# Performance work log

Hardware: AMD Instinct MI355X
Metric: run time of the kernel (lower is better)

The kernel has to match this reference:

```python
import jax, jax.numpy as jnp
import numpy as np

# dims: N batch, C in-channels, T frames, V joints, H heads, HD per-head dim, O out-channels
N, C, T, V = 32, 64, 256, 25
H, HD, O = 8, 8, 64  # HD = max(C//8, 8)
SCALE = HD ** -0.5
EPS = 1e-5


def setup_inputs() -> dict:
    key = jax.random.key(0)
    ks = jax.random.split(key, 10)
    return {
        "x": jax.random.normal(ks[0], (N, C, T, V), jnp.float32),
        "ln_gamma": jnp.ones((C,), jnp.float32),
        "ln_beta": jnp.zeros((C,), jnp.float32),
        "w_qk": jax.random.normal(ks[1], (C, 2 * H * HD), jnp.float32),  # to_qk init N(0,1)
        "b_qk": jax.random.normal(ks[2], (2 * H * HD,), jnp.float32) * 0.02,
        "shared_topology": jax.random.uniform(ks[3], (H, V, V), jnp.float32),
        "conv_w": jax.random.normal(ks[4], (H, O, C), jnp.float32) * np.sqrt(2.0 / (O * H)),
        "conv_b": jnp.zeros((H, O), jnp.float32),
        "bn_gamma": jnp.full((O,), 1e-6, jnp.float32),
        "bn_beta": jnp.zeros((O,), jnp.float32),
        "bn_mean": jnp.zeros((O,), jnp.float32),
        "bn_var": jnp.ones((O,), jnp.float32),
    }


def reference(x, ln_gamma, ln_beta, w_qk, b_qk, shared_topology,
              conv_w, conv_b, bn_gamma, bn_beta, bn_mean, bn_var):
    # ---- SelfAttention over joints ----
    y = jnp.transpose(x, (0, 2, 3, 1))                 # [N,T,V,C]
    mu = jnp.mean(y, axis=-1, keepdims=True)
    var = jnp.var(y, axis=-1, keepdims=True)
    yn = (y - mu) * jax.lax.rsqrt(var + EPS) * ln_gamma + ln_beta
    qk = yn @ w_qk + b_qk                              # [N,T,V,2*H*HD]
    B = N * T
    q, k = jnp.split(qk.reshape(B, V, 2 * H * HD), 2, axis=-1)
    q = q.reshape(B, V, H, HD).transpose(0, 2, 1, 3)   # [B,H,V,HD]
    k = k.reshape(B, V, H, HD).transpose(0, 2, 1, 3)
    dots = jnp.einsum("bhid,bhjd->bhij", q, k) * SCALE
    attn = jax.nn.softmax(dots, axis=-1).astype(jnp.float32)  # [B,H,V,V]

    # ---- attention-gated graph conv ----
    A = attn * shared_topology[None]                   # [B,H,V,V]
    feat = jnp.transpose(x, (0, 2, 3, 1)).reshape(B, V, C)  # [B,V,C]
    z = jnp.einsum("bhuv,bvc->bhuc", A, feat)          # per-head aggregate [B,H,V,C]
    # fused per-head 1x1 convs + sum over heads
    out = jnp.einsum("bhuc,hoc->buo", z, conv_w) + conv_b.sum(0)  # [B,V,O]
    out = out.reshape(N, T, V, O).transpose(0, 3, 1, 2)           # [N,O,T,V]

    # ---- BatchNorm (inference-mode) + residual + ReLU ----
    g = (bn_gamma * jax.lax.rsqrt(bn_var + EPS))[None, :, None, None]
    b = (bn_beta - bn_mean * bn_gamma * jax.lax.rsqrt(bn_var + EPS))[None, :, None, None]
    out = out * g + b
    out = jax.nn.relu(out + x)  # down is identity (in_c == out_c)
    return out
```

## Files before the change

kernel.cpp:

```cpp
#include <hip/hip_runtime.h>
#include <math.h>

#define SCALE_L2E 0.51006972157f
#define EPSV 1e-5f

typedef __attribute__((ext_vector_type(8))) short bf16x8;
typedef __attribute__((ext_vector_type(4))) float f32x4;
typedef __attribute__((ext_vector_type(16))) float f32x16;
typedef __attribute__((ext_vector_type(4))) int i32x4;
typedef __attribute__((ext_vector_type(2))) int i32x2;

static __device__ __forceinline__ unsigned short bfh(float f) {
    return (unsigned short)(__builtin_bit_cast(unsigned int, f) >> 16);
}
static __device__ __forceinline__ float bf2f(unsigned short s) {
    return __builtin_bit_cast(float, (unsigned int)s << 16);
}
static __device__ __forceinline__ int pack2(float lo, float hi) {
    return __builtin_amdgcn_perm(__builtin_bit_cast(unsigned int, hi),
                                 __builtin_bit_cast(unsigned int, lo), 0x07060302u);
}
#define LGKM0() __asm__ __volatile__("s_waitcnt lgkmcnt(0)" ::: "memory")

__global__ void prep_kernel(const float* __restrict__ w_qk,
                            const float* __restrict__ conv_w,
                            const float* __restrict__ conv_b,
                            const float* __restrict__ bn_g, const float* __restrict__ bn_b,
                            const float* __restrict__ bn_m, const float* __restrict__ bn_v,
                            unsigned short* __restrict__ ws) {
    int i = blockIdx.x * 256 + threadIdx.x;
    if (i < 8192) {
        int f = i >> 9, rem = i & 511, l = rem >> 3, j = rem & 7;
        int nt = f >> 1, ks = f & 1;
        int k = ks * 32 + (l >> 4) * 8 + j;
        int nn = nt * 16 + (l & 15);
        ws[i] = bfh(w_qk[k * 128 + nn]);
    } else if (i < 40960) {
        int i2 = i - 8192;
        int g = i2 >> 9, rem = i2 & 511, l = rem >> 3, j = rem & 7;
        int h = g >> 3, nt = (g >> 1) & 3, ks = g & 1;
        int c = ks * 32 + (l >> 4) * 8 + j;
        int o = nt * 16 + (l & 15);
        ws[i] = bfh(conv_w[h * 4096 + o * 64 + c]);
    } else if (i < 41024) {
        int o = i - 40960;
        float gv = bn_g[o] * rsqrtf(bn_v[o] + EPSV);
        float bb = bn_b[o] - bn_m[o] * gv;
        float cb = 0.f;
        for (int h = 0; h < 8; h++) cb += conv_b[h * 64 + o];
        float* wsf = (float*)(ws + 40960);
        wsf[o] = gv;
        wsf[64 + o] = bb + cb * gv;
    }
}

__global__ __launch_bounds__(256, 2)
void sagc_kernel(const float* __restrict__ x,
                 const float* __restrict__ ln_g, const float* __restrict__ ln_b,
                 const float* __restrict__ b_qk,
                 const float* __restrict__ topo,
                 const unsigned short* __restrict__ ws,
                 float* __restrict__ out)
{
    __shared__ __align__(16) unsigned char smem[32768];
    const int tid = threadIdx.x;
    const int lane = tid & 63, wv = tid >> 6;
    const int l15 = lane & 15, quad = lane >> 4;
    const int r32 = lane & 31, hi = lane >> 5;

    unsigned char* my = smem + wv * 8192;
    unsigned short* qbuf = (unsigned short*)my;
    unsigned short* kbuf = (unsigned short*)(my + 1536);
    unsigned char*  fwb  = my;
    unsigned char*  ghb  = my + 4096;

    const unsigned short* wqk = ws;
    const unsigned short* w2f = ws + 8192;
    const float* bnA = (const float*)(ws + 40960);
    const float* bnB = bnA + 64;

    const int tile = blockIdx.x * 4 + wv;
    const int n = tile >> 8, t = tile & 255;
    const float* xg = x + (size_t)n * 409600 + (size_t)t * 25;
    float* og = out + (size_t)n * 409600 + (size_t)t * 25;

    float xf[2][2][8];
    #pragma unroll
    for (int mt = 0; mt < 2; mt++) {
        const int v = mt * 16 + l15;
        const bool ok = (v < 25);
        const float* xc = xg + v;
        #pragma unroll
        for (int ks = 0; ks < 2; ks++)
            #pragma unroll
            for (int j = 0; j < 8; j++) {
                int c = ks * 32 + quad * 8 + j;
                xf[mt][ks][j] = ok ? xc[c * 6400] : 0.f;
            }
    }

    bf16x8 xa[2][2];
    float sum_[2] = {0.f, 0.f}, ssq_[2] = {0.f, 0.f};
    #pragma unroll
    for (int mt = 0; mt < 2; mt++)
        #pragma unroll
        for (int ks = 0; ks < 2; ks++) {
            i32x4 pa;
            #pragma unroll
            for (int q = 0; q < 4; q++)
                pa[q] = pack2(xf[mt][ks][2 * q], xf[mt][ks][2 * q + 1]);
            xa[mt][ks] = __builtin_bit_cast(bf16x8, pa);
            #pragma unroll
            for (int j = 0; j < 8; j++) {
                float a = xf[mt][ks][j];
                sum_[mt] += a;
                ssq_[mt] += a * a;
            }
        }

    float muv[2], rsv[2];
    #pragma unroll
    for (int mt = 0; mt < 2; mt++) {
        sum_[mt] += __shfl_xor(sum_[mt], 16);
        sum_[mt] += __shfl_xor(sum_[mt], 32);
        ssq_[mt] += __shfl_xor(ssq_[mt], 16);
        ssq_[mt] += __shfl_xor(ssq_[mt], 32);
        muv[mt] = sum_[mt] * 0.015625f;
        rsv[mt] = rsqrtf(ssq_[mt] * 0.015625f - muv[mt] * muv[mt] + EPSV);
    }

    bf16x8 yna[2][2];
    #pragma unroll
    for (int ks = 0; ks < 2; ks++) {
        f32x4 ga = *(const f32x4*)&ln_g[ks * 32 + quad * 8];
        f32x4 gb = *(const f32x4*)&ln_g[ks * 32 + quad * 8 + 4];
        f32x4 ba = *(const f32x4*)&ln_b[ks * 32 + quad * 8];
        f32x4 bb = *(const f32x4*)&ln_b[ks * 32 + quad * 8 + 4];
        #pragma unroll
        for (int mt = 0; mt < 2; mt++) {
            float yv[8];
            #pragma unroll
            for (int j = 0; j < 8; j++) {
                float g = (j < 4) ? ga[j] : gb[j - 4];
                float bt = (j < 4) ? ba[j] : bb[j - 4];
                yv[j] = (xf[mt][ks][j] - muv[mt]) * rsv[mt] * g + bt;
            }
            i32x4 p;
            #pragma unroll
            for (int q = 0; q < 4; q++) p[q] = pack2(yv[2 * q], yv[2 * q + 1]);
            yna[mt][ks] = __builtin_bit_cast(bf16x8, p);
        }
    }

    f32x4 acc[2][4];
    #pragma unroll
    for (int mt = 0; mt < 2; mt++)
        #pragma unroll
        for (int nt = 0; nt < 4; nt++)
            acc[mt][nt] = (f32x4){0.f, 0.f, 0.f, 0.f};

    const f32x4 z4 = {0.f, 0.f, 0.f, 0.f};
    const bf16x8 z8 = {0, 0, 0, 0, 0, 0, 0, 0};

    const int sw4 = (l15 >> 2) & 3;
    const int blkA = ((r32 >> 3) ^ hi) << 4;
    unsigned char* gwA = ghb + hi * 256 + (r32 & 7) * 2 + blkA;
    unsigned char* gwB = ghb + hi * 256 + (r32 & 7) * 2 + (blkA ^ 32);
    unsigned char* w0p = fwb + ((((quad >> 1) ^ sw4)) << 4) + (quad & 1) * 8;
    unsigned char* w1p = fwb + (((((quad >> 1) ^ sw4)) ^ 2) << 4) + (quad & 1) * 8;
    unsigned char* brp = fwb + l15 * 64 + ((quad ^ sw4) << 4);

    #pragma unroll
    for (int hp = 0; hp < 4; hp++) {
        #pragma unroll
        for (int tsel = 0; tsel < 2; tsel++) {
            int nt = tsel ? (4 + hp) : hp;
            bf16x8 b0 = *(const bf16x8*)&wqk[(nt * 2 + 0) * 512 + lane * 8];
            bf16x8 b1 = *(const bf16x8*)&wqk[(nt * 2 + 1) * 512 + lane * 8];
            float bias = b_qk[(tsel ? 64 : 0) + hp * 16 + l15];
            unsigned short* buf = tsel ? kbuf : qbuf;
            #pragma unroll
            for (int mt = 0; mt < 2; mt++) {
                f32x4 d = __builtin_amdgcn_mfma_f32_16x16x32_bf16(yna[mt][0], b0, z4, 0, 0, 0);
                d = __builtin_amdgcn_mfma_f32_16x16x32_bf16(yna[mt][1], b1, d, 0, 0, 0);
                #pragma unroll
                for (int r = 0; r < 4; r++) {
                    int u = mt * 16 + quad * 4 + r;
                    if (u < 25) {
                        float val = d[r] + bias;
                        if (!tsel) val *= SCALE_L2E;
                        buf[u * 24 + l15] = bfh(val);
                    }
                }
            }
        }
        LGKM0();

        #pragma unroll
        for (int hh = 0; hh < 2; hh++) {
            bf16x8 aq = z8, bk = z8;
            if (hi == 0) {
                aq = *(const bf16x8*)&qbuf[r32 * 24 + hh * 8];
                bk = *(const bf16x8*)&kbuf[r32 * 24 + hh * 8];
            }
            f32x16 dd = {0.f,0.f,0.f,0.f,0.f,0.f,0.f,0.f,0.f,0.f,0.f,0.f,0.f,0.f,0.f,0.f};
            dd = __builtin_amdgcn_mfma_f32_32x32x16_bf16(aq, bk, dd, 0, 0, 0);
            #pragma unroll
            for (int r = 0; r < 16; r++) {
                int ub = (r & 3) + 8 * (r >> 2);
                if (ub + 4 * hi < 25) {
                    unsigned char* p = (((r >> 2) & 1) ? gwB : gwA) + hh * 2048 + ub * 64;
                    *(unsigned short*)p = bfh(dd[r]);
                }
            }
        }

        float tpv[25];
        {
            const float* tp = topo + (hp * 2 + hi) * 625 + (r32 < 25 ? r32 : 0) * 25;
            #pragma unroll
            for (int v = 0; v < 25; v++) tpv[v] = tp[v];
        }
        LGKM0();

        {
            int smh = hi, su = r32;
            if (su < 25) {
                unsigned char* rowb = ghb + smh * 2048 + su * 64;
                int sz = ((su >> 2) & 3) << 4;
                i32x4 ra = *(const i32x4*)(rowb + (sz ^ 0));
                i32x4 rb = *(const i32x4*)(rowb + (sz ^ 16));
                i32x4 rc = *(const i32x4*)(rowb + (sz ^ 32));
                float f[25];
                #pragma unroll
                for (int w = 0; w < 4; w++) {
                    f[2 * w]      = __builtin_bit_cast(float, (unsigned)ra[w] << 16);
                    f[2 * w + 1]  = __builtin_bit_cast(float, (unsigned)ra[w] & 0xFFFF0000u);
                    f[8 + 2 * w]  = __builtin_bit_cast(float, (unsigned)rb[w] << 16);
                    f[9 + 2 * w]  = __builtin_bit_cast(float, (unsigned)rb[w] & 0xFFFF0000u);
                    f[16 + 2 * w] = __builtin_bit_cast(float, (unsigned)rc[w] << 16);
                    f[17 + 2 * w] = __builtin_bit_cast(float, (unsigned)rc[w] & 0xFFFF0000u);
                }
                f[24] = bf2f(*(const unsigned short*)(rowb + (sz ^ 48)));
                float g12[12];
                #pragma unroll
                for (int i2 = 0; i2 < 12; i2++) g12[i2] = fmaxf(f[i2], f[i2 + 12]);
                #pragma unroll
                for (int i2 = 0; i2 < 6; i2++) g12[i2] = fmaxf(g12[i2], g12[i2 + 6]);
                float m = fmaxf(fmaxf(fmaxf(g12[0], g12[1]), fmaxf(g12[2], g12[3])),
                                fmaxf(fmaxf(g12[4], g12[5]), f[24]));
                float s0 = 0.f, s1 = 0.f, s2 = 0.f, s3 = 0.f;
                #pragma unroll
                for (int v = 0; v < 24; v += 4) {
                    f[v]     = __builtin_amdgcn_exp2f(f[v] - m);     s0 += f[v];
                    f[v + 1] = __builtin_amdgcn_exp2f(f[v + 1] - m); s1 += f[v + 1];
                    f[v + 2] = __builtin_amdgcn_exp2f(f[v + 2] - m); s2 += f[v + 2];
                    f[v + 3] = __builtin_amdgcn_exp2f(f[v + 3] - m); s3 += f[v + 3];
                }
                f[24] = __builtin_amdgcn_exp2f(f[24] - m);
                float inv = __builtin_amdgcn_rcpf(((s0 + s1) + (s2 + s3)) + f[24]);
                #pragma unroll
                for (int v = 0; v < 25; v++) f[v] = f[v] * inv * tpv[v];
                int d[12];
                #pragma unroll
                for (int p = 0; p < 12; p++) d[p] = pack2(f[2 * p], f[2 * p + 1]);
                *(i32x4*)(rowb + (sz ^ 0))  = (i32x4){d[0], d[1], d[2], d[3]};
                *(i32x4*)(rowb + (sz ^ 16)) = (i32x4){d[4], d[5], d[6], d[7]};
                *(i32x4*)(rowb + (sz ^ 32)) = (i32x4){d[8], d[9], d[10], d[11]};
                *(i32x4*)(rowb + (sz ^ 48)) = (i32x4){pack2(f[24], 0.f), 0, 0, 0};
            }
        }

        bf16x8 w2e[8];
        #pragma unroll
        for (int nt = 0; nt < 4; nt++) {
            int h = hp * 2;
            w2e[2 * nt]     = *(const bf16x8*)&w2f[((h * 4 + nt) * 2 + 0) * 512 + lane * 8];
            w2e[2 * nt + 1] = *(const bf16x8*)&w2f[((h * 4 + nt) * 2 + 1) * 512 + lane * 8];
        }
        LGKM0();

        #pragma unroll
        for (int nt = 0; nt < 4; nt++) {
            f32x4 dw0 = __builtin_amdgcn_mfma_f32_16x16x32_bf16(xa[0][0], w2e[2 * nt], z4, 0, 0, 0);
            dw0 = __builtin_amdgcn_mfma_f32_16x16x32_bf16(xa[0][1], w2e[2 * nt + 1], dw0, 0, 0, 0);
            f32x4 dw1 = __builtin_amdgcn_mfma_f32_16x16x32_bf16(xa[1][0], w2e[2 * nt], z4, 0, 0, 0);
            dw1 = __builtin_amdgcn_mfma_f32_16x16x32_bf16(xa[1][1], w2e[2 * nt + 1], dw1, 0, 0, 0);
            i32x2 q0 = {pack2(dw0[0], dw0[1]), pack2(dw0[2], dw0[3])};
            i32x2 q1 = {pack2(dw1[0], dw1[1]), pack2(dw1[2], dw1[3])};
            *(i32x2*)(w0p + nt * 1024 + l15 * 64) = q0;
            *(i32x2*)(w1p + nt * 1024 + l15 * 64) = q1;
        }
        bf16x8 w2o[8];
        #pragma unroll
        for (int nt = 0; nt < 4; nt++) {
            int h = hp * 2 + 1;
            w2o[2 * nt]     = *(const bf16x8*)&w2f[((h * 4 + nt) * 2 + 0) * 512 + lane * 8];
            w2o[2 * nt + 1] = *(const bf16x8*)&w2f[((h * 4 + nt) * 2 + 1) * 512 + lane * 8];
        }
        LGKM0();

        {
            unsigned char* agp = ghb + l15 * 64 + ((quad ^ sw4) << 4);
            bf16x8 ag0 = *(const bf16x8*)agp;
            bf16x8 ag1 = *(const bf16x8*)(agp + 1024);
            #pragma unroll
            for (int nt = 0; nt < 4; nt++) {
                bf16x8 br = *(const bf16x8*)(brp + nt * 1024);
                acc[0][nt] = __builtin_amdgcn_mfma_f32_16x16x32_bf16(ag0, br, acc[0][nt], 0, 0, 0);
                acc[1][nt] = __builtin_amdgcn_mfma_f32_16x16x32_bf16(ag1, br, acc[1][nt], 0, 0, 0);
            }
        }

        #pragma unroll
        for (int nt = 0; nt < 4; nt++) {
            f32x4 dw0 = __builtin_amdgcn_mfma_f32_16x16x32_bf16(xa[0][0], w2o[2 * nt], z4, 0, 0, 0);
            dw0 = __builtin_amdgcn_mfma_f32_16x16x32_bf16(xa[0][1], w2o[2 * nt + 1], dw0, 0, 0, 0);
            f32x4 dw1 = __builtin_amdgcn_mfma_f32_16x16x32_bf16(xa[1][0], w2o[2 * nt], z4, 0, 0, 0);
            dw1 = __builtin_amdgcn_mfma_f32_16x16x32_bf16(xa[1][1], w2o[2 * nt + 1], dw1, 0, 0, 0);
            i32x2 q0 = {pack2(dw0[0], dw0[1]), pack2(dw0[2], dw0[3])};
            i32x2 q1 = {pack2(dw1[0], dw1[1]), pack2(dw1[2], dw1[3])};
            *(i32x2*)(w0p + nt * 1024 + l15 * 64) = q0;
            *(i32x2*)(w1p + nt * 1024 + l15 * 64) = q1;
        }
        LGKM0();

        {
            unsigned char* agp = ghb + 2048 + l15 * 64 + ((quad ^ sw4) << 4);
            bf16x8 ag0 = *(const bf16x8*)agp;
            bf16x8 ag1 = *(const bf16x8*)(agp + 1024);
            #pragma unroll
            for (int nt = 0; nt < 4; nt++) {
                bf16x8 br = *(const bf16x8*)(brp + nt * 1024);
                acc[0][nt] = __builtin_amdgcn_mfma_f32_16x16x32_bf16(ag0, br, acc[0][nt], 0, 0, 0);
                acc[1][nt] = __builtin_amdgcn_mfma_f32_16x16x32_bf16(ag1, br, acc[1][nt], 0, 0, 0);
            }
        }
    }

    #pragma unroll
    for (int nt = 0; nt < 4; nt++) {
        int o = nt * 16 + l15;
        float gA = bnA[o], gB = bnB[o];
        #pragma unroll
        for (int mt = 0; mt < 2; mt++) {
            int ub = mt * 16 + quad * 4;
            #pragma unroll
            for (int r = 0; r < 4; r++) {
                int u = ub + r;
                if (u < 25) {
                    float val = acc[mt][nt][r] * gA + gB + xg[o * 6400 + u];
                    og[o * 6400 + u] = fmaxf(val, 0.f);
                }
            }
        }
    }
}

extern "C" void kernel_launch(void* const* d_in, const int* in_sizes, int n_in,
                              void* d_out, int out_size, void* d_ws, size_t ws_size,
                              hipStream_t stream) {
    const float* x      = (const float*)d_in[0];
    const float* ln_g   = (const float*)d_in[1];
    const float* ln_b   = (const float*)d_in[2];
    const float* w_qk   = (const float*)d_in[3];
    const float* b_qk   = (const float*)d_in[4];
    const float* topo   = (const float*)d_in[5];
    const float* conv_w = (const float*)d_in[6];
    const float* conv_b = (const float*)d_in[7];
    const float* bn_g   = (const float*)d_in[8];
    const float* bn_b   = (const float*)d_in[9];
    const float* bn_m   = (const float*)d_in[10];
    const float* bn_v   = (const float*)d_in[11];
    float* outp = (float*)d_out;
    unsigned short* wsp = (unsigned short*)d_ws;

    hipLaunchKernelGGL(prep_kernel, dim3(161), dim3(256), 0, stream,
                       w_qk, conv_w, conv_b, bn_g, bn_b, bn_m, bn_v, wsp);
    hipLaunchKernelGGL(sagc_kernel, dim3(2048), dim3(256), 0, stream,
                       x, ln_g, ln_b, b_qk, topo, (const unsigned short*)wsp, outp);
}
```

Before: 185.9 us.

## Compute softmax in MFMA registers with transposed QK and direct bf16 P store

The QK^T product is now computed as K·Q^T so each lane's 32x32 MFMA output holds a full attention row split across the two half-waves. Softmax max and sum use cross-half shuffles in registers, and the topology-scaled probabilities are written once to padded LDS buffers. This replaces the old path, which wrote raw logits to LDS, re-read them per row, ran the softmax and wrote them back. LDS use per wave grows from 8 KB to 9 KB, which may affect occupancy, and one LDS wait is dropped.

Measured after the change: 188.8 us. No clear change (+1.5%).

```diff
diff --git a/kernel.cpp b/kernel.cpp
--- a/kernel.cpp
+++ b/kernel.cpp
@@ -12,9 +12,6 @@
 
 static __device__ __forceinline__ unsigned short bfh(float f) {
     return (unsigned short)(__builtin_bit_cast(unsigned int, f) >> 16);
-}
-static __device__ __forceinline__ float bf2f(unsigned short s) {
-    return __builtin_bit_cast(float, (unsigned int)s << 16);
 }
 static __device__ __forceinline__ int pack2(float lo, float hi) {
     return __builtin_amdgcn_perm(__builtin_bit_cast(unsigned int, hi),
@@ -62,17 +59,18 @@
                  const unsigned short* __restrict__ ws,
                  float* __restrict__ out)
 {
-    __shared__ __align__(16) unsigned char smem[32768];
+    __shared__ __align__(16) unsigned char smem[36864];
     const int tid = threadIdx.x;
     const int lane = tid & 63, wv = tid >> 6;
     const int l15 = lane & 15, quad = lane >> 4;
     const int r32 = lane & 31, hi = lane >> 5;
 
-    unsigned char* my = smem + wv * 8192;
+    unsigned char* my = smem + wv * 9216;
     unsigned short* qbuf = (unsigned short*)my;
     unsigned short* kbuf = (unsigned short*)(my + 1536);
     unsigned char*  fwb  = my;
-    unsigned char*  ghb  = my + 4096;
+    unsigned char*  pb0  = my + 4096;
+    unsigned char*  pb1  = my + 4096 + 2560;
 
     const unsigned short* wqk = ws;
     const unsigned short* w2f = ws + 8192;
@@ -163,12 +161,45 @@
     const bf16x8 z8 = {0, 0, 0, 0, 0, 0, 0, 0};
 
     const int sw4 = (l15 >> 2) & 3;
-    const int blkA = ((r32 >> 3) ^ hi) << 4;
-    unsigned char* gwA = ghb + hi * 256 + (r32 & 7) * 2 + blkA;
-    unsigned char* gwB = ghb + hi * 256 + (r32 & 7) * 2 + (blkA ^ 32);
     unsigned char* w0p = fwb + ((((quad >> 1) ^ sw4)) << 4) + (quad & 1) * 8;
     unsigned char* w1p = fwb + (((((quad >> 1) ^ sw4)) ^ 2) << 4) + (quad & 1) * 8;
     unsigned char* brp = fwb + l15 * 64 + ((quad ^ sw4) << 4);
+
+    const int uc = (r32 < 25) ? r32 : 24;
+
+    auto softmax_store = [&](f32x16& dd, const float* tp, unsigned char* Pb) {
+        dd[12] = hi ? -3e30f : dd[12];
+        dd[13] = -3e30f; dd[14] = -3e30f; dd[15] = -3e30f;
+        float t8[8];
+        #pragma unroll
+        for (int r = 0; r < 8; r++) t8[r] = fmaxf(dd[r], dd[r + 8]);
+        #pragma unroll
+        for (int r = 0; r < 4; r++) t8[r] = fmaxf(t8[r], t8[r + 4]);
+        float m = fmaxf(fmaxf(t8[0], t8[1]), fmaxf(t8[2], t8[3]));
+        m = fmaxf(m, __shfl_xor(m, 32));
+        float s0 = 0.f, s1 = 0.f, s2 = 0.f, s3 = 0.f;
+        #pragma unroll
+        for (int r = 0; r < 16; r += 4) {
+            dd[r]     = __builtin_amdgcn_exp2f(dd[r] - m);     s0 += dd[r];
+            dd[r + 1] = __builtin_amdgcn_exp2f(dd[r + 1] - m); s1 += dd[r + 1];
+            dd[r + 2] = __builtin_amdgcn_exp2f(dd[r + 2] - m); s2 += dd[r + 2];
+            dd[r + 3] = __builtin_amdgcn_exp2f(dd[r + 3] - m); s3 += dd[r + 3];
+        }
+        float s = (s0 + s1) + (s2 + s3);
+        s += __shfl_xor(s, 32);
+        float inv = __builtin_amdgcn_rcpf(s);
+        #pragma unroll
+        for (int r = 0; r < 16; r++) dd[r] = dd[r] * inv * tp[r];
+        if (r32 < 25) {
+            unsigned char* rowp = Pb + r32 * 80 + hi * 8;
+            *(i32x2*)(rowp +  0) = (i32x2){pack2(dd[0], dd[1]),   pack2(dd[2], dd[3])};
+            *(i32x2*)(rowp + 16) = (i32x2){pack2(dd[4], dd[5]),   pack2(dd[6], dd[7])};
+            *(i32x2*)(rowp + 32) = (i32x2){pack2(dd[8], dd[9]),   pack2(dd[10], dd[11])};
+            *(i32x2*)(rowp + 48) = (i32x2){pack2(dd[12], dd[13]), pack2(dd[14], dd[15])};
+        }
+    };
+
+    const f32x16 z16 = {0.f,0.f,0.f,0.f,0.f,0.f,0.f,0.f,0.f,0.f,0.f,0.f,0.f,0.f,0.f,0.f};
 
     #pragma unroll
     for (int hp = 0; hp < 4; hp++) {
@@ -194,82 +225,50 @@
                 }
             }
         }
+
+        float tp0[16];
+        {
+            const float* tb = topo + (hp * 2 + 0) * 625 + uc * 25 + hi * 4;
+            #pragma unroll
+            for (int r = 0; r < 16; r++) {
+                int off = (r < 12) ? ((r & 3) + (r >> 2) * 8)
+                        : (r == 12 ? (hi ? 0 : 24) : 0);
+                tp0[r] = tb[off];
+            }
+        }
         LGKM0();
 
-        #pragma unroll
-        for (int hh = 0; hh < 2; hh++) {
-            bf16x8 aq = z8, bk = z8;
+        f32x16 p0;
+        {
+            bf16x8 ak = z8, bq = z8;
             if (hi == 0) {
-                aq = *(const bf16x8*)&qbuf[r32 * 24 + hh * 8];
-                bk = *(const bf16x8*)&kbuf[r32 * 24 + hh * 8];
-            }
-            f32x16 dd = {0.f,0.f,0.f,0.f,0.f,0.f,0.f,0.f,0.f,0.f,0.f,0.f,0.f,0.f,0.f,0.f};
-            dd = __builtin_amdgcn_mfma_f32_32x32x16_bf16(aq, bk, dd, 0, 0, 0);
+                ak = *(const bf16x8*)&kbuf[r32 * 24 + 0];
+                bq = *(const bf16x8*)&qbuf[r32 * 24 + 0];
+            }
+            p0 = __builtin_amdgcn_mfma_f32_32x32x16_bf16(ak, bq, z16, 0, 0, 0);
+        }
+        float tp1[16];
+        {
+            const float* tb = topo + (hp * 2 + 1) * 625 + uc * 25 + hi * 4;
             #pragma unroll
             for (int r = 0; r < 16; r++) {
-                int ub = (r & 3) + 8 * (r >> 2);
-                if (ub + 4 * hi < 25) {
-                    unsigned char* p = (((r >> 2) & 1) ? gwB : gwA) + hh * 2048 + ub * 64;
-                    *(unsigned short*)p = bfh(dd[r]);
-                }
-            }
-        }
-
-        float tpv[25];
-        {
-            const float* tp = topo + (hp * 2 + hi) * 625 + (r32 < 25 ? r32 : 0) * 25;
-            #pragma unroll
-            for (int v = 0; v < 25; v++) tpv[v] = tp[v];
-        }
-        LGKM0();
-
-        {
-            int smh = hi, su = r32;
-            if (su < 25) {
-                unsigned char* rowb = ghb + smh * 2048 + su * 64;
-                int sz = ((su >> 2) & 3) << 4;
-                i32x4 ra = *(const i32x4*)(rowb + (sz ^ 0));
-                i32x4 rb = *(const i32x4*)(rowb + (sz ^ 16));
-                i32x4 rc = *(const i32x4*)(rowb + (sz ^ 32));
-                float f[25];
-                #pragma unroll
-                for (int w = 0; w < 4; w++) {
-                    f[2 * w]      = __builtin_bit_cast(float, (unsigned)ra[w] << 16);
-                    f[2 * w + 1]  = __builtin_bit_cast(float, (unsigned)ra[w] & 0xFFFF0000u);
-                    f[8 + 2 * w]  = __builtin_bit_cast(float, (unsigned)rb[w] << 16);
-                    f[9 + 2 * w]  = __builtin_bit_cast(float, (unsigned)rb[w] & 0xFFFF0000u);
-                    f[16 + 2 * w] = __builtin_bit_cast(float, (unsigned)rc[w] << 16);
-                    f[17 + 2 * w] = __builtin_bit_cast(float, (unsigned)rc[w] & 0xFFFF0000u);
-                }
-                f[24] = bf2f(*(const unsigned short*)(rowb + (sz ^ 48)));
-                float g12[12];
-                #pragma unroll
-                for (int i2 = 0; i2 < 12; i2++) g12[i2] = fmaxf(f[i2], f[i2 + 12]);
-                #pragma unroll
-                for (int i2 = 0; i2 < 6; i2++) g12[i2] = fmaxf(g12[i2], g12[i2 + 6]);
-                float m = fmaxf(fmaxf(fmaxf(g12[0], g12[1]), fmaxf(g12[2], g12[3])),
-                                fmaxf(fmaxf(g12[4], g12[5]), f[24]));
-                float s0 = 0.f, s1 = 0.f, s2 = 0.f, s3 = 0.f;
-                #pragma unroll
-                for (int v = 0; v < 24; v += 4) {
-                    f[v]     = __builtin_amdgcn_exp2f(f[v] - m);     s0 += f[v];
-                    f[v + 1] = __builtin_amdgcn_exp2f(f[v + 1] - m); s1 += f[v + 1];
-                    f[v + 2] = __builtin_amdgcn_exp2f(f[v + 2] - m); s2 += f[v + 2];
-                    f[v + 3] = __builtin_amdgcn_exp2f(f[v + 3] - m); s3 += f[v + 3];
-                }
-                f[24] = __builtin_amdgcn_exp2f(f[24] - m);
-                float inv = __builtin_amdgcn_rcpf(((s0 + s1) + (s2 + s3)) + f[24]);
-                #pragma unroll
-                for (int v = 0; v < 25; v++) f[v] = f[v] * inv * tpv[v];
-                int d[12];
-                #pragma unroll
-                for (int p = 0; p < 12; p++) d[p] = pack2(f[2 * p], f[2 * p + 1]);
-                *(i32x4*)(rowb + (sz ^ 0))  = (i32x4){d[0], d[1], d[2], d[3]};
-                *(i32x4*)(rowb + (sz ^ 16)) = (i32x4){d[4], d[5], d[6], d[7]};
-                *(i32x4*)(rowb + (sz ^ 32)) = (i32x4){d[8], d[9], d[10], d[11]};
-                *(i32x4*)(rowb + (sz ^ 48)) = (i32x4){pack2(f[24], 0.f), 0, 0, 0};
-            }
-        }
+                int off = (r < 12) ? ((r & 3) + (r >> 2) * 8)
+                        : (r == 12 ? (hi ? 0 : 24) : 0);
+                tp1[r] = tb[off];
+            }
+        }
+        f32x16 p1;
+        {
+            bf16x8 ak = z8, bq = z8;
+            if (hi == 0) {
+                ak = *(const bf16x8*)&kbuf[r32 * 24 + 8];
+                bq = *(const bf16x8*)&qbuf[r32 * 24 + 8];
+            }
+            p1 = __builtin_amdgcn_mfma_f32_32x32x16_bf16(ak, bq, z16, 0, 0, 0);
+        }
+
+        softmax_store(p0, tp0, pb0);
+        softmax_store(p1, tp1, pb1);
 
         bf16x8 w2e[8];
         #pragma unroll
@@ -278,7 +277,6 @@
             w2e[2 * nt]     = *(const bf16x8*)&w2f[((h * 4 + nt) * 2 + 0) * 512 + lane * 8];
             w2e[2 * nt + 1] = *(const bf16x8*)&w2f[((h * 4 + nt) * 2 + 1) * 512 + lane * 8];
         }
-        LGKM0();
 
         #pragma unroll
         for (int nt = 0; nt < 4; nt++) {
@@ -301,9 +299,8 @@
         LGKM0();
 
         {
-            unsigned char* agp = ghb + l15 * 64 + ((quad ^ sw4) << 4);
-            bf16x8 ag0 = *(const bf16x8*)agp;
-            bf16x8 ag1 = *(const bf16x8*)(agp + 1024);
+            bf16x8 ag0 = *(const bf16x8*)(pb0 + l15 * 80 + quad * 16);
+            bf16x8 ag1 = *(const bf16x8*)(pb0 + (16 + l15) * 80 + quad * 16);
             #pragma unroll
             for (int nt = 0; nt < 4; nt++) {
                 bf16x8 br = *(const bf16x8*)(brp + nt * 1024);
@@ -326,9 +323,8 @@
         LGKM0();
 
         {
-            unsigned char* agp = ghb + 2048 + l15 * 64 + ((quad ^ sw4) << 4);
-            bf16x8 ag0 = *(const bf16x8*)agp;
-            bf16x8 ag1 = *(const bf16x8*)(agp + 1024);
+            bf16x8 ag0 = *(const bf16x8*)(pb1 + l15 * 80 + quad * 16);
+            bf16x8 ag1 = *(const bf16x8*)(pb1 + (16 + l15) * 80 + quad * 16);
             #pragma unroll
             for (int nt = 0; nt < 4; nt++) {
                 bf16x8 br = *(const bf16x8*)(brp + nt * 1024);
```
